# Kernel tuning notes

Hardware: AMD Instinct MI355X
Metric: run time of the kernel (lower is better)

The kernel has to match this reference:

```python
import jax, jax.numpy as jnp
import numpy as np

D_MODEL = 4096
NUM_EXPERTS = 64
TOP_K = 2


def setup_inputs() -> dict:
    key = jax.random.key(0)
    kx, kw, kb = jax.random.split(key, 3)
    x = jax.random.normal(kx, (4, 4096, D_MODEL), dtype=jnp.float32)
    # nn.Linear(d_model, num_experts): weight [E, D], bias [E]
    bound = 1.0 / np.sqrt(D_MODEL)
    W = jax.random.uniform(kw, (NUM_EXPERTS, D_MODEL), dtype=jnp.float32, minval=-bound, maxval=bound)
    b = jax.random.uniform(kb, (NUM_EXPERTS,), dtype=jnp.float32, minval=-bound, maxval=bound)
    return {"x": x, "W": W, "b": b}


def reference(x, W, b):
    # logits = gate(x): [B, S, E]
    logits = jnp.einsum("bsd,ed->bse", x, W) + b
    scores = jax.nn.softmax(logits, axis=-1)
    topk_scores, topk_idx = jax.lax.top_k(scores, TOP_K)  # [B,S,K]
    # scatter top-k scores back into a dense [B,S,E] dispatch mask
    onehot = jax.nn.one_hot(topk_idx, NUM_EXPERTS, dtype=scores.dtype)  # [B,S,K,E]
    dispatch_mask = jnp.einsum("bske,bsk->bse", onehot, topk_scores)
    return dispatch_mask
```

## Files before the change

### kernel.cpp

```cpp
#include <hip/hip_runtime.h>
#include <hip/hip_bf16.h>
#include <math.h>
#include <stdint.h>

#define DM 4096
#define NEXP 64
#define BK 64
#define NCH (DM / BK)
#define TOKW 32
#define KSPLIT 8
#define CHPS (NCH / KSPLIT)

typedef short bf16x8 __attribute__((ext_vector_type(8)));
typedef float f32x4  __attribute__((ext_vector_type(4)));

__device__ __forceinline__ void split2(float f0, float f1, uint32_t& hw, uint32_t& lw) {
    float2 ff; ff.x = f0; ff.y = f1;
    __hip_bfloat162 h = __float22bfloat162_rn(ff);
    union { __hip_bfloat162 b; uint32_t u; } ch; ch.b = h;
    hw = ch.u;
    float h0 = __bfloat162float(h.x);
    float h1 = __bfloat162float(h.y);
    float2 gg; gg.x = f0 - h0; gg.y = f1 - h1;
    __hip_bfloat162 l = __float22bfloat162_rn(gg);
    union { __hip_bfloat162 b; uint32_t u; } cl; cl.b = l;
    lw = cl.u;
}

__global__ __launch_bounds__(128) void wsplit_kernel(const float* __restrict__ W,
                                                     char* __restrict__ blob) {
    const int c   = blockIdx.x;
    const int eq  = blockIdx.y;
    const int tid = threadIdx.x;
    const int e   = eq * 16 + (tid >> 3);
    const int g   = tid & 7;

    const float* src = W + (size_t)e * DM + c * BK + g * 8;
    float x[8];
    *(float4*)(x)     = *(const float4*)(src);
    *(float4*)(x + 4) = *(const float4*)(src + 4);

    uint32_t hiw[4], low[4];
#pragma unroll
    for (int j = 0; j < 4; ++j) split2(x[2 * j], x[2 * j + 1], hiw[j], low[j]);

    const int ks = g >> 2;
    const int ln = (e & 15) | ((g & 3) << 4);
    const int n4 = e >> 4;
    const size_t base = (size_t)c * 16384 + (size_t)ks * 4096 + (size_t)n4 * 1024 + (size_t)ln * 16;
    *(uint4*)(blob + base)        = *(uint4*)hiw;
    *(uint4*)(blob + base + 8192) = *(uint4*)low;
}

__global__ __launch_bounds__(512, 4) void router_mfma_kernel(
    const float* __restrict__ X,
    const char* __restrict__ blob,
    const float* __restrict__ Bv,
    float* __restrict__ out)
{
    __shared__ float part[KSPLIT][TOKW][NEXP];

    const int tid  = threadIdx.x;
    const int lane = tid & 63;
    const int wv   = tid >> 6;
    const long tok0 = (long)blockIdx.x * TOKW;

    const int tk = lane & 15;
    const int kg = lane >> 4;

    const float* a0 = X + (size_t)(tok0 + tk) * DM + (size_t)wv * (CHPS * BK) + kg * 8;
    const float* a1 = a0 + (size_t)16 * DM;
    const char*  bw = blob + (size_t)(wv * CHPS) * 16384;

    f32x4 acc[2][4];
#pragma unroll
    for (int m = 0; m < 2; ++m)
#pragma unroll
        for (int n = 0; n < 4; ++n) acc[m][n] = (f32x4)0.0f;

#pragma unroll 1
    for (int ci = 0; ci < CHPS; ++ci) {
        const char* bb = bw + (size_t)ci * 16384;

        float ar[2][2][8];
#pragma unroll
        for (int m = 0; m < 2; ++m) {
            const float* am = (m == 0) ? a0 : a1;
#pragma unroll
            for (int ks = 0; ks < 2; ++ks) {
                const float* p = am + ci * BK + ks * 32;
                *(float4*)(ar[m][ks])     = *(const float4*)(p);
                *(float4*)(ar[m][ks] + 4) = *(const float4*)(p + 4);
            }
        }

        bf16x8 ah[2][2], al[2][2];
#pragma unroll
        for (int m = 0; m < 2; ++m)
#pragma unroll
            for (int ks = 0; ks < 2; ++ks) {
                uint32_t hw[4], lw[4];
#pragma unroll
                for (int j = 0; j < 4; ++j)
                    split2(ar[m][ks][2 * j], ar[m][ks][2 * j + 1], hw[j], lw[j]);
                ah[ks][m] = *(bf16x8*)hw;
                al[ks][m] = *(bf16x8*)lw;
            }

#pragma unroll
        for (int ks = 0; ks < 2; ++ks) {
#pragma unroll
            for (int n = 0; n < 4; ++n) {
                const size_t bo = (size_t)ks * 4096 + (size_t)n * 1024 + (size_t)lane * 16;
                bf16x8 bh = *(const bf16x8*)(bb + bo);
                bf16x8 bl = *(const bf16x8*)(bb + 8192 + bo);
#pragma unroll
                for (int m = 0; m < 2; ++m) {
                    acc[m][n] = __builtin_amdgcn_mfma_f32_16x16x32_bf16(ah[ks][m], bh, acc[m][n], 0, 0, 0);
                    acc[m][n] = __builtin_amdgcn_mfma_f32_16x16x32_bf16(ah[ks][m], bl, acc[m][n], 0, 0, 0);
                    acc[m][n] = __builtin_amdgcn_mfma_f32_16x16x32_bf16(al[ks][m], bh, acc[m][n], 0, 0, 0);
                }
            }
        }
    }

#pragma unroll
    for (int m = 0; m < 2; ++m)
#pragma unroll
        for (int n = 0; n < 4; ++n)
#pragma unroll
            for (int r = 0; r < 4; ++r)
                part[wv][m * 16 + kg * 4 + r][n * 16 + tk] = acc[m][n][r];
    __syncthreads();

#pragma unroll
    for (int i = 0; i < 4; ++i) {
        const int cell = tid + i * 512;
        const int t = cell >> 6;
        const int e = cell & 63;
        float s = part[0][t][e];
#pragma unroll
        for (int w = 1; w < KSPLIT; ++w) s += part[w][t][e];
        part[0][t][e] = s;
    }
    __syncthreads();

    const float bias = Bv[lane];
#pragma unroll 1
    for (int j = 0; j < TOKW / KSPLIT; ++j) {
        const int t = wv * (TOKW / KSPLIT) + j;
        float v = part[0][t][lane] + bias;

        float m1 = v;        int i1 = lane;
        float m2 = -3.4e38f; int i2 = 127;
#pragma unroll
        for (int s = 1; s < 64; s <<= 1) {
            float om1 = __shfl_xor(m1, s, 64);
            int   oi1 = __shfl_xor(i1, s, 64);
            float om2 = __shfl_xor(m2, s, 64);
            int   oi2 = __shfl_xor(i2, s, 64);
            bool bw2 = (om1 > m1) || (om1 == m1 && oi1 < i1);
            float l1v = bw2 ? m1 : om1;  int l1i = bw2 ? i1 : oi1;
            float w2v = bw2 ? om2 : m2;  int w2i = bw2 ? oi2 : i2;
            if (bw2) { m1 = om1; i1 = oi1; }
            bool tw = (l1v > w2v) || (l1v == w2v && l1i < w2i);
            m2 = tw ? l1v : w2v;  i2 = tw ? l1i : w2i;
        }

        float p = expf(v - m1);
        float ssum = p;
#pragma unroll
        for (int s = 1; s < 64; s <<= 1) ssum += __shfl_xor(ssum, s, 64);

        float sc = (lane == i1 || lane == i2) ? (p / ssum) : 0.0f;
        out[(size_t)(tok0 + t) * NEXP + lane] = sc;
    }
}

extern "C" void kernel_launch(void* const* d_in, const int* in_sizes, int n_in,
                              void* d_out, int out_size, void* d_ws, size_t ws_size,
                              hipStream_t stream) {
    const float* X  = (const float*)d_in[0];
    const float* W  = (const float*)d_in[1];
    const float* Bv = (const float*)d_in[2];
    float* out = (float*)d_out;

    char* blob = (char*)d_ws;
    wsplit_kernel<<<dim3(NCH, 4), dim3(128), 0, stream>>>(W, blob);

    const int n_tokens = 4 * 4096;
    router_mfma_kernel<<<dim3(n_tokens / TOKW), dim3(512), 0, stream>>>(X, blob, Bv, out);
}
```

Before: 74.84 us.

## Halve tokens per block to one MFMA row tile and raise occupancy

Cuts each block from 32 to 16 tokens, so each wave holds one M-tile of accumulators instead of two. This halves register and LDS use, lets launch bounds ask for 6 blocks per CU, and doubles the grid size. The LDS partial buffer is padded to 66 columns to reduce bank conflicts. In exchange, each B-fragment load from the split weight blob now feeds only one M-tile, so weight traffic per token doubles.

New measurement: 95.71 us. 27.9% more time.

```diff
diff --git a/kernel.cpp b/kernel.cpp
--- a/kernel.cpp
+++ b/kernel.cpp
@@ -7,7 +7,7 @@
 #define NEXP 64
 #define BK 64
 #define NCH (DM / BK)
-#define TOKW 32
+#define TOKW 16
 #define KSPLIT 8
 #define CHPS (NCH / KSPLIT)
 
@@ -52,13 +52,13 @@
     *(uint4*)(blob + base + 8192) = *(uint4*)low;
 }
 
-__global__ __launch_bounds__(512, 4) void router_mfma_kernel(
+__global__ __launch_bounds__(512, 6) void router_mfma_kernel(
     const float* __restrict__ X,
     const char* __restrict__ blob,
     const float* __restrict__ Bv,
     float* __restrict__ out)
 {
-    __shared__ float part[KSPLIT][TOKW][NEXP];
+    __shared__ float part[KSPLIT][TOKW][66];
 
     const int tid  = threadIdx.x;
     const int lane = tid & 63;
@@ -69,43 +69,34 @@
     const int kg = lane >> 4;
 
     const float* a0 = X + (size_t)(tok0 + tk) * DM + (size_t)wv * (CHPS * BK) + kg * 8;
-    const float* a1 = a0 + (size_t)16 * DM;
     const char*  bw = blob + (size_t)(wv * CHPS) * 16384;
 
-    f32x4 acc[2][4];
+    f32x4 acc[4];
 #pragma unroll
-    for (int m = 0; m < 2; ++m)
-#pragma unroll
-        for (int n = 0; n < 4; ++n) acc[m][n] = (f32x4)0.0f;
+    for (int n = 0; n < 4; ++n) acc[n] = (f32x4)0.0f;
 
 #pragma unroll 1
     for (int ci = 0; ci < CHPS; ++ci) {
         const char* bb = bw + (size_t)ci * 16384;
 
-        float ar[2][2][8];
+        float ar[2][8];
 #pragma unroll
-        for (int m = 0; m < 2; ++m) {
-            const float* am = (m == 0) ? a0 : a1;
-#pragma unroll
-            for (int ks = 0; ks < 2; ++ks) {
-                const float* p = am + ci * BK + ks * 32;
-                *(float4*)(ar[m][ks])     = *(const float4*)(p);
-                *(float4*)(ar[m][ks] + 4) = *(const float4*)(p + 4);
-            }
+        for (int ks = 0; ks < 2; ++ks) {
+            const float* p = a0 + ci * BK + ks * 32;
+            *(float4*)(ar[ks])     = *(const float4*)(p);
+            *(float4*)(ar[ks] + 4) = *(const float4*)(p + 4);
         }
 
-        bf16x8 ah[2][2], al[2][2];
+        bf16x8 ah[2], al[2];
 #pragma unroll
-        for (int m = 0; m < 2; ++m)
+        for (int ks = 0; ks < 2; ++ks) {
+            uint32_t hw[4], lw[4];
 #pragma unroll
-            for (int ks = 0; ks < 2; ++ks) {
-                uint32_t hw[4], lw[4];
-#pragma unroll
-                for (int j = 0; j < 4; ++j)
-                    split2(ar[m][ks][2 * j], ar[m][ks][2 * j + 1], hw[j], lw[j]);
-                ah[ks][m] = *(bf16x8*)hw;
-                al[ks][m] = *(bf16x8*)lw;
-            }
+            for (int j = 0; j < 4; ++j)
+                split2(ar[ks][2 * j], ar[ks][2 * j + 1], hw[j], lw[j]);
+            ah[ks] = *(bf16x8*)hw;
+            al[ks] = *(bf16x8*)lw;
+        }
 
 #pragma unroll
         for (int ks = 0; ks < 2; ++ks) {
@@ -114,27 +105,22 @@
                 const size_t bo = (size_t)ks * 4096 + (size_t)n * 1024 + (size_t)lane * 16;
                 bf16x8 bh = *(const bf16x8*)(bb + bo);
                 bf16x8 bl = *(const bf16x8*)(bb + 8192 + bo);
-#pragma unroll
-                for (int m = 0; m < 2; ++m) {
-                    acc[m][n] = __builtin_amdgcn_mfma_f32_16x16x32_bf16(ah[ks][m], bh, acc[m][n], 0, 0, 0);
-                    acc[m][n] = __builtin_amdgcn_mfma_f32_16x16x32_bf16(ah[ks][m], bl, acc[m][n], 0, 0, 0);
-                    acc[m][n] = __builtin_amdgcn_mfma_f32_16x16x32_bf16(al[ks][m], bh, acc[m][n], 0, 0, 0);
-                }
+                acc[n] = __builtin_amdgcn_mfma_f32_16x16x32_bf16(ah[ks], bh, acc[n], 0, 0, 0);
+                acc[n] = __builtin_amdgcn_mfma_f32_16x16x32_bf16(ah[ks], bl, acc[n], 0, 0, 0);
+                acc[n] = __builtin_amdgcn_mfma_f32_16x16x32_bf16(al[ks], bh, acc[n], 0, 0, 0);
             }
         }
     }
 
 #pragma unroll
-    for (int m = 0; m < 2; ++m)
+    for (int n = 0; n < 4; ++n)
 #pragma unroll
-        for (int n = 0; n < 4; ++n)
-#pragma unroll
-            for (int r = 0; r < 4; ++r)
-                part[wv][m * 16 + kg * 4 + r][n * 16 + tk] = acc[m][n][r];
+        for (int r = 0; r < 4; ++r)
+            part[wv][kg * 4 + r][n * 16 + tk] = acc[n][r];
     __syncthreads();
 
 #pragma unroll
-    for (int i = 0; i < 4; ++i) {
+    for (int i = 0; i < 2; ++i) {
         const int cell = tid + i * 512;
         const int t = cell >> 6;
         const int e = cell & 63;
```
